# Kernel tuning notes

Hardware: AMD Instinct MI355X
Metric: run time of the kernel (lower is better)

Reference implementation:

```python
import jax, jax.numpy as jnp
import numpy as np

B, S, D = 4, 2048, 1024
H = 16
HD = D // H  # head_dim = 64


def setup_inputs() -> dict:
    key = jax.random.key(0)
    ks = jax.random.split(key, 8)
    scale = 1.0 / np.sqrt(D)
    return {
        "X_Q": jax.random.normal(ks[0], (B, S, D), dtype=jnp.float32),
        "X_KV": jax.random.normal(ks[1], (B, S, D), dtype=jnp.float32),
        # q_proj: Linear(D, D), weights stored as (in, out)
        "q_w": jax.random.normal(ks[2], (D, D), dtype=jnp.float32) * scale,
        "q_b": jax.random.normal(ks[3], (D,), dtype=jnp.float32) * scale,
        # kv_proj: Linear(D, 2*D)
        "kv_w": jax.random.normal(ks[4], (D, 2 * D), dtype=jnp.float32) * scale,
        "kv_b": jax.random.normal(ks[5], (2 * D,), dtype=jnp.float32) * scale,
        # out_proj: Linear(D, D) (query_dim == input_dim)
        "out_w": jax.random.normal(ks[6], (D, D), dtype=jnp.float32) * scale,
        "out_b": jax.random.normal(ks[7], (D,), dtype=jnp.float32) * scale,
    }


def reference(X_Q, X_KV, q_w, q_b, kv_w, kv_b, out_w, out_b):
    # projections
    q = X_Q @ q_w + q_b                      # [b, s, D]
    kv = X_KV @ kv_w + kv_b                  # [b, l, 2D]
    k, v = jnp.split(kv, 2, axis=-1)         # each [b, l, D]

    def split_heads(t):
        b, m, _ = t.shape
        return t.reshape(b, m, H, HD).transpose(0, 2, 1, 3)  # [b, h, m, d]

    q, k, v = split_heads(q), split_heads(k), split_heads(v)

    # standard attention: full SxL scores (non-flash path)
    scores = jnp.einsum("bhsd,bhld->bhsl", q, k) / np.sqrt(HD)
    attn = jax.nn.softmax(scores, axis=-1)   # dropout_p = 0 -> identity
    out = jnp.einsum("bhsl,bhld->bhsd", attn, v)

    # merge heads: [b, h, s, d] -> [b, s, h*d]
    out = out.transpose(0, 2, 1, 3).reshape(B, S, D)
    return out @ out_w + out_b
```

## Files before the change

### kernel.cpp

```cpp
#include <hip/hip_runtime.h>
#include <hip/hip_bf16.h>
#include <math.h>

#define B_  4
#define S_  2048
#define D_  1024
#define H_  16
#define HD_ 64

typedef __bf16 bf16;
typedef __bf16 bf16x4 __attribute__((ext_vector_type(4)));
typedef __bf16 bf16x8 __attribute__((ext_vector_type(8)));
typedef float  floatx4 __attribute__((ext_vector_type(4)));

#define QSCALE 0.18033688011112042f

__device__ __forceinline__ void async_load16(const bf16* g, bf16* l) {
  __builtin_amdgcn_global_load_lds(
      (const __attribute__((address_space(1))) void*)g,
      (__attribute__((address_space(3))) void*)l, 16, 0, 0);
}

__global__ __launch_bounds__(256) void prep_all(
    const float* __restrict__ xa, bf16* __restrict__ oa,
    const float* __restrict__ xb, bf16* __restrict__ ob,
    const float* __restrict__ qw, bf16* __restrict__ qwT,
    const float* __restrict__ kvw, bf16* __restrict__ kvwT,
    const float* __restrict__ ow, bf16* __restrict__ owT) {
  __shared__ float tile[32][33];
  int bid = blockIdx.x;
  if (bid < 16384) {
    const float* in; bf16* out; int i;
    if (bid < 8192) { in = xa; out = oa; i = (bid * 256 + threadIdx.x) * 4; }
    else            { in = xb; out = ob; i = ((bid - 8192) * 256 + threadIdx.x) * 4; }
    float4 v = *reinterpret_cast<const float4*>(in + i);
    bf16x4 o;
    o[0] = (bf16)v.x; o[1] = (bf16)v.y; o[2] = (bf16)v.z; o[3] = (bf16)v.w;
    *reinterpret_cast<bf16x4*>(out + i) = o;
    return;
  }
  bid -= 16384;
  const float* in; bf16* out; int N, lb;
  if (bid < 1024)      { in = qw;  out = qwT;  N = 1024; lb = bid; }
  else if (bid < 3072) { in = kvw; out = kvwT; N = 2048; lb = bid - 1024; }
  else                 { in = ow;  out = owT;  N = 1024; lb = bid - 3072; }
  int nx = N >> 5;
  int n0 = (lb % nx) * 32, k0 = (lb / nx) * 32;
  int tx = threadIdx.x & 31, ty = threadIdx.x >> 5;
  #pragma unroll
  for (int i = ty; i < 32; i += 8)
    tile[i][tx] = in[(size_t)(k0 + i) * N + n0 + tx];
  __syncthreads();
  #pragma unroll
  for (int i = ty; i < 32; i += 8)
    out[(size_t)(n0 + i) * 1024 + k0 + tx] = (bf16)tile[tx][i];
}

template <int MODE>
__device__ __forceinline__ void gemm_body(
    const bf16* __restrict__ A, const bf16* __restrict__ Bt,
    const float* __restrict__ bias, void* __restrict__ out,
    int M, int N, int K, int bx, int by,
    bf16 (*As)[64], bf16 (*Bs)[64]) {
  const int tid  = threadIdx.x;
  const int m0   = by * 128;
  const int n0   = bx * 128;
  const int w    = tid >> 6;
  const int lane = tid & 63;
  const int lr   = lane & 15;
  const int lq   = lane >> 4;
  const int wm   = (w >> 1) * 64;
  const int wn   = (w & 1) * 64;

  const int srow = lane >> 3;
  const int sg   = (lane & 7) ^ srow;
  const bf16* aptr = A  + (size_t)(m0 + 32 * w + srow) * K + 8 * sg;
  const bf16* bptr = Bt + (size_t)(n0 + 32 * w + srow) * K + 8 * sg;

  floatx4 acc[4][4];
  #pragma unroll
  for (int i = 0; i < 4; i++)
    #pragma unroll
    for (int j = 0; j < 4; j++)
      acc[i][j] = floatx4{0.f, 0.f, 0.f, 0.f};

  for (int k0 = 0; k0 < K; k0 += 64) {
    __syncthreads();
    #pragma unroll
    for (int p = 0; p < 4; p++) {
      async_load16(aptr + (size_t)8 * p * K + k0, &As[32 * w + 8 * p][0]);
      async_load16(bptr + (size_t)8 * p * K + k0, &Bs[32 * w + 8 * p][0]);
    }
    __syncthreads();
    #pragma unroll
    for (int kc = 0; kc < 2; kc++) {
      const int sw = 8 * ((kc * 4 + lq) ^ (lr & 7));
      bf16x8 af[4], bfv[4];
      #pragma unroll
      for (int t = 0; t < 4; t++)
        af[t] = *reinterpret_cast<const bf16x8*>(&As[wm + 16 * t + lr][sw]);
      #pragma unroll
      for (int t = 0; t < 4; t++)
        bfv[t] = *reinterpret_cast<const bf16x8*>(&Bs[wn + 16 * t + lr][sw]);
      #pragma unroll
      for (int i = 0; i < 4; i++)
        #pragma unroll
        for (int j = 0; j < 4; j++)
          acc[i][j] = __builtin_amdgcn_mfma_f32_16x16x32_bf16(af[i], bfv[j], acc[i][j], 0, 0, 0);
    }
  }

  #pragma unroll
  for (int i = 0; i < 4; i++) {
    int row_base = m0 + wm + 16 * i + lq * 4;
    #pragma unroll
    for (int j = 0; j < 4; j++) {
      int col = n0 + wn + 16 * j + lr;
      float bv = bias[col];
      if (MODE == 2 && col >= 1024) {
        int b = row_base >> 11, s0 = row_base & 2047;
        int c = col - 1024, h = c >> 6, d = c & 63;
        bf16* Vt = (bf16*)out + (size_t)B_ * H_ * S_ * HD_;
        bf16x4 pk;
        #pragma unroll
        for (int r = 0; r < 4; r++) pk[r] = (bf16)(acc[i][j][r] + bv);
        *reinterpret_cast<bf16x4*>(
            &Vt[(((size_t)b * H_ + h) * HD_ + d) * S_ + s0]) = pk;
        continue;
      }
      #pragma unroll
      for (int r = 0; r < 4; r++) {
        int row = row_base + r;
        float v = acc[i][j][r] + bv;
        if (MODE == 0) {
          ((float*)out)[(size_t)row * N + col] = v;
        } else if (MODE == 1) {
          int b = row >> 11, s = row & 2047;
          int h = col >> 6, d = col & 63;
          ((bf16*)out)[(((size_t)b * H_ + h) * S_ + s) * HD_ + d] =
              (bf16)(v * QSCALE);
        } else {
          int b = row >> 11, s = row & 2047;
          int h = col >> 6, d = col & 63;
          ((bf16*)out)[(((size_t)b * H_ + h) * S_ + s) * HD_ + d] = (bf16)v;
        }
      }
    }
  }
}

__global__ __launch_bounds__(256) void gemm_out(
    const bf16* __restrict__ A, const bf16* __restrict__ Bt,
    const float* __restrict__ bias, void* __restrict__ out,
    int M, int N, int K) {
  __shared__ bf16 As[128][64];
  __shared__ bf16 Bs[128][64];
  gemm_body<0>(A, Bt, bias, out, M, N, K, blockIdx.x, blockIdx.y, As, Bs);
}

__global__ __launch_bounds__(256) void gemm_qkv(
    const bf16* __restrict__ Xq, const bf16* __restrict__ qwT,
    const float* __restrict__ q_b, bf16* __restrict__ Qb,
    const bf16* __restrict__ Xkv, const bf16* __restrict__ kvwT,
    const float* __restrict__ kv_b, bf16* __restrict__ KVb) {
  __shared__ bf16 As[128][64];
  __shared__ bf16 Bs[128][64];
  int bid = blockIdx.x;
  if (bid < 512) {
    gemm_body<1>(Xq, qwT, q_b, Qb, 8192, 1024, 1024, bid & 7, bid >> 3, As, Bs);
  } else {
    int b2 = bid - 512;
    gemm_body<2>(Xkv, kvwT, kv_b, KVb, 8192, 2048, 1024, b2 & 15, b2 >> 4, As, Bs);
  }
}

__global__ __launch_bounds__(256, 2) void attn_kernel(
    const bf16* __restrict__ Q, const bf16* __restrict__ Kb,
    const bf16* __restrict__ Vt, bf16* __restrict__ out) {
  __shared__ bf16 smem[8192];

  const int tid  = threadIdx.x;
  const int w    = tid >> 6;
  const int lane = tid & 63;
  const int lr   = lane & 15;
  const int lq   = lane >> 4;
  const int bh   = blockIdx.x;
  const int q0   = blockIdx.y * 256;
  const size_t base = (size_t)bh * S_ * HD_;

  bf16* pw = smem + w * 2048;

  const bf16* kit = Kb + base + (size_t)lr * HD_ + 8 * lq;
  const bf16* vit = Vt + base + (size_t)lr * S_ + 8 * lq;

  bf16x8 bq[4][2];
  #pragma unroll
  for (int g = 0; g < 4; g++) {
    const bf16* qrow = Q + base + (size_t)(q0 + 64 * w + 16 * g + lr) * HD_;
    bq[g][0] = *reinterpret_cast<const bf16x8*>(qrow + lq * 8);
    bq[g][1] = *reinterpret_cast<const bf16x8*>(qrow + 32 + lq * 8);
  }

  const int plx = lr >> 1;

  float l_i[4] = {0.f, 0.f, 0.f, 0.f};
  floatx4 o_acc[4][4];
  #pragma unroll
  for (int g = 0; g < 4; g++)
    #pragma unroll
    for (int t = 0; t < 4; t++) o_acc[g][t] = floatx4{0.f, 0.f, 0.f, 0.f};

  const int NIT = S_ / 64;
  for (int it = 0; it < NIT; it++) {
    auto qkt = [&](int t) {
      bf16x8 ak0 = *reinterpret_cast<const bf16x8*>(kit + 16 * t * HD_);
      bf16x8 ak1 = *reinterpret_cast<const bf16x8*>(kit + 16 * t * HD_ + 32);
      floatx4 sc[4];
      #pragma unroll
      for (int g = 0; g < 4; g++) {
        sc[g] = __builtin_amdgcn_mfma_f32_16x16x32_bf16(ak0, bq[g][0],
                    floatx4{0.f, 0.f, 0.f, 0.f}, 0, 0, 0);
        sc[g] = __builtin_amdgcn_mfma_f32_16x16x32_bf16(ak1, bq[g][1], sc[g], 0, 0, 0);
      }
      const int pcol = 4 * ((4 * (t & 1) + lq) ^ plx);
      #pragma unroll
      for (int g = 0; g < 4; g++) {
        bf16x4 pk;
        float lsum = 0.f;
        #pragma unroll
        for (int r = 0; r < 4; r++) {
          float p = __builtin_amdgcn_exp2f(sc[g][r]);
          lsum += p;
          pk[r] = (bf16)p;
        }
        l_i[g] += lsum;
        *reinterpret_cast<bf16x4*>(&pw[(16 * g + lr) * 32 + pcol]) = pk;
      }
    };

    auto pv = [&](const bf16x8* av) {
      bf16x8 bp[4];
      #pragma unroll
      for (int g = 0; g < 4; g++) {
        union { bf16x4 h[2]; bf16x8 v; } f;
        f.h[0] = *reinterpret_cast<const bf16x4*>(
            &pw[(16 * g + lr) * 32 + 4 * ((2 * lq + 0) ^ plx)]);
        f.h[1] = *reinterpret_cast<const bf16x4*>(
            &pw[(16 * g + lr) * 32 + 4 * ((2 * lq + 1) ^ plx)]);
        bp[g] = f.v;
      }
      __builtin_amdgcn_s_setprio(1);
      #pragma unroll
      for (int t2 = 0; t2 < 4; t2++)
        #pragma unroll
        for (int g = 0; g < 4; g++)
          o_acc[g][t2] = __builtin_amdgcn_mfma_f32_16x16x32_bf16(av[t2], bp[g], o_acc[g][t2], 0, 0, 0);
      __builtin_amdgcn_s_setprio(0);
    };

    bf16x8 av0[4];
    #pragma unroll
    for (int t2 = 0; t2 < 4; t2++)
      av0[t2] = *reinterpret_cast<const bf16x8*>(vit + (size_t)16 * t2 * S_);
    qkt(0);
    qkt(1);
    __builtin_amdgcn_wave_barrier();
    pv(av0);
    __builtin_amdgcn_wave_barrier();
    bf16x8 av1[4];
    #pragma unroll
    for (int t2 = 0; t2 < 4; t2++)
      av1[t2] = *reinterpret_cast<const bf16x8*>(vit + (size_t)16 * t2 * S_ + 32);
    qkt(2);
    qkt(3);
    __builtin_amdgcn_wave_barrier();
    pv(av1);

    kit += 64 * HD_;
    vit += 64;
  }

  #pragma unroll
  for (int g = 0; g < 4; g++) {
    l_i[g] += __shfl_xor(l_i[g], 16, 64);
    l_i[g] += __shfl_xor(l_i[g], 32, 64);
  }

  const int b = bh >> 4, h = bh & 15;
  #pragma unroll
  for (int g = 0; g < 4; g++) {
    const float inv = 1.0f / l_i[g];
    const int qrow = q0 + 64 * w + 16 * g + lr;
    bf16* orow = out + ((size_t)b * S_ + qrow) * D_ + h * HD_;
    #pragma unroll
    for (int t = 0; t < 4; t++) {
      bf16x4 pk;
      #pragma unroll
      for (int r = 0; r < 4; r++) pk[r] = (bf16)(o_acc[g][t][r] * inv);
      *reinterpret_cast<bf16x4*>(&orow[16 * t + lq * 4]) = pk;
    }
  }
}

extern "C" void kernel_launch(void* const* d_in, const int* in_sizes, int n_in,
                              void* d_out, int out_size, void* d_ws, size_t ws_size,
                              hipStream_t stream) {
  const float* X_Q   = (const float*)d_in[0];
  const float* X_KV  = (const float*)d_in[1];
  const float* q_w   = (const float*)d_in[2];
  const float* q_b   = (const float*)d_in[3];
  const float* kv_w  = (const float*)d_in[4];
  const float* kv_b  = (const float*)d_in[5];
  const float* out_w = (const float*)d_in[6];
  const float* out_b = (const float*)d_in[7];
  float* out = (float*)d_out;

  char* ws = (char*)d_ws;
  const size_t MB = 1024 * 1024;
  bf16* Xq   = (bf16*)(ws + 0);
  bf16* Xkv  = (bf16*)(ws + 16 * MB);
  bf16* Qb   = (bf16*)(ws + 32 * MB);
  bf16* Kb   = (bf16*)(ws + 48 * MB);
  bf16* qwT  = (bf16*)(ws + 80 * MB);
  bf16* kvwT = (bf16*)(ws + 82 * MB);
  bf16* owT  = (bf16*)(ws + 86 * MB);
  bf16* Vt   = Kb + (size_t)B_ * H_ * S_ * HD_;
  bf16* attn = Xq;

  prep_all<<<20480, 256, 0, stream>>>(X_Q, Xq, X_KV, Xkv,
                                      q_w, qwT, kv_w, kvwT, out_w, owT);
  gemm_qkv<<<1536, 256, 0, stream>>>(Xq, qwT, q_b, Qb, Xkv, kvwT, kv_b, Kb);
  attn_kernel<<<dim3(64, 8), 256, 0, stream>>>(Qb, Kb, Vt, attn);
  gemm_out<<<dim3(8, 64), 256, 0, stream>>>(attn, owT, out_b, out, 8192, 1024, 1024);
}
```

Measured before the change: 343.7 us.

## Prefetch K tiles into registers and swap MFMA operands for vectorized GEMM stores

The attention loop now loads the next iteration's K fragments into a second register set while computing on the current one, hiding global load latency behind the QK^T and PV MFMAs. The GEMMs gain a SWAP mode that exchanges the MFMA operands, so each lane holds four consecutive output columns. The epilogue can then use a vector bias load and 16-byte float or 8-byte bf16 stores instead of scalar writes. The cost is extra registers in the attention kernel, which could reduce occupancy under the 2-block launch bound.

```diff
diff --git a/kernel.cpp b/kernel.cpp
--- a/kernel.cpp
+++ b/kernel.cpp
@@ -56,7 +56,7 @@
     out[(size_t)(n0 + i) * 1024 + k0 + tx] = (bf16)tile[tx][i];
 }
 
-template <int MODE>
+template <int MODE, bool SWAP>
 __device__ __forceinline__ void gemm_body(
     const bf16* __restrict__ A, const bf16* __restrict__ Bt,
     const float* __restrict__ bias, void* __restrict__ out,
@@ -105,9 +105,41 @@
       #pragma unroll
       for (int i = 0; i < 4; i++)
         #pragma unroll
-        for (int j = 0; j < 4; j++)
-          acc[i][j] = __builtin_amdgcn_mfma_f32_16x16x32_bf16(af[i], bfv[j], acc[i][j], 0, 0, 0);
-    }
+        for (int j = 0; j < 4; j++) {
+          if (SWAP)
+            acc[i][j] = __builtin_amdgcn_mfma_f32_16x16x32_bf16(bfv[i], af[j], acc[i][j], 0, 0, 0);
+          else
+            acc[i][j] = __builtin_amdgcn_mfma_f32_16x16x32_bf16(af[i], bfv[j], acc[i][j], 0, 0, 0);
+        }
+    }
+  }
+
+  if (SWAP) {
+    #pragma unroll
+    for (int i = 0; i < 4; i++) {
+      const int colb = n0 + wn + 16 * i + 4 * lq;
+      const floatx4 bv4 = *reinterpret_cast<const floatx4*>(&bias[colb]);
+      #pragma unroll
+      for (int j = 0; j < 4; j++) {
+        const int row = m0 + wm + 16 * j + lr;
+        if (MODE == 0) {
+          floatx4 v = acc[i][j] + bv4;
+          *reinterpret_cast<floatx4*>(&((float*)out)[(size_t)row * N + colb]) = v;
+        } else {
+          const int b = row >> 11, s = row & 2047;
+          const int h = colb >> 6, d0 = colb & 63;
+          bf16x4 pk;
+          #pragma unroll
+          for (int r = 0; r < 4; r++) {
+            float v = acc[i][j][r] + bv4[r];
+            pk[r] = (bf16)(MODE == 1 ? v * QSCALE : v);
+          }
+          *reinterpret_cast<bf16x4*>(
+              &((bf16*)out)[(((size_t)b * H_ + h) * S_ + s) * HD_ + d0]) = pk;
+        }
+      }
+    }
+    return;
   }
 
   #pragma unroll
@@ -134,15 +166,11 @@
         float v = acc[i][j][r] + bv;
         if (MODE == 0) {
           ((float*)out)[(size_t)row * N + col] = v;
-        } else if (MODE == 1) {
+        } else {
           int b = row >> 11, s = row & 2047;
           int h = col >> 6, d = col & 63;
           ((bf16*)out)[(((size_t)b * H_ + h) * S_ + s) * HD_ + d] =
-              (bf16)(v * QSCALE);
-        } else {
-          int b = row >> 11, s = row & 2047;
-          int h = col >> 6, d = col & 63;
-          ((bf16*)out)[(((size_t)b * H_ + h) * S_ + s) * HD_ + d] = (bf16)v;
+              (bf16)(MODE == 1 ? v * QSCALE : v);
         }
       }
     }
@@ -155,7 +183,7 @@
     int M, int N, int K) {
   __shared__ bf16 As[128][64];
   __shared__ bf16 Bs[128][64];
-  gemm_body<0>(A, Bt, bias, out, M, N, K, blockIdx.x, blockIdx.y, As, Bs);
+  gemm_body<0, true>(A, Bt, bias, out, M, N, K, blockIdx.x, blockIdx.y, As, Bs);
 }
 
 __global__ __launch_bounds__(256) void gemm_qkv(
@@ -167,10 +195,14 @@
   __shared__ bf16 Bs[128][64];
   int bid = blockIdx.x;
   if (bid < 512) {
-    gemm_body<1>(Xq, qwT, q_b, Qb, 8192, 1024, 1024, bid & 7, bid >> 3, As, Bs);
+    gemm_body<1, true>(Xq, qwT, q_b, Qb, 8192, 1024, 1024, bid & 7, bid >> 3, As, Bs);
   } else {
     int b2 = bid - 512;
-    gemm_body<2>(Xkv, kvwT, kv_b, KVb, 8192, 2048, 1024, b2 & 15, b2 >> 4, As, Bs);
+    int bx = b2 & 15, by = b2 >> 4;
+    if (bx < 8)
+      gemm_body<2, true>(Xkv, kvwT, kv_b, KVb, 8192, 2048, 1024, bx, by, As, Bs);
+    else
+      gemm_body<2, false>(Xkv, kvwT, kv_b, KVb, 8192, 2048, 1024, bx, by, As, Bs);
   }
 }
 
@@ -211,16 +243,32 @@
     for (int t = 0; t < 4; t++) o_acc[g][t] = floatx4{0.f, 0.f, 0.f, 0.f};
 
   const int NIT = S_ / 64;
-  for (int it = 0; it < NIT; it++) {
+
+  bf16x8 kA[8], kB[8];
+  #pragma unroll
+  for (int t = 0; t < 4; t++) {
+    kA[2 * t]     = *reinterpret_cast<const bf16x8*>(kit + 16 * t * HD_);
+    kA[2 * t + 1] = *reinterpret_cast<const bf16x8*>(kit + 16 * t * HD_ + 32);
+  }
+  kit += 64 * HD_;
+
+  auto body = [&](bf16x8 (&cur)[8], bf16x8 (&nxt)[8], int it) {
+    if (it + 1 < NIT) {
+      #pragma unroll
+      for (int t = 0; t < 4; t++) {
+        nxt[2 * t]     = *reinterpret_cast<const bf16x8*>(kit + 16 * t * HD_);
+        nxt[2 * t + 1] = *reinterpret_cast<const bf16x8*>(kit + 16 * t * HD_ + 32);
+      }
+      kit += 64 * HD_;
+    }
+
     auto qkt = [&](int t) {
-      bf16x8 ak0 = *reinterpret_cast<const bf16x8*>(kit + 16 * t * HD_);
-      bf16x8 ak1 = *reinterpret_cast<const bf16x8*>(kit + 16 * t * HD_ + 32);
       floatx4 sc[4];
       #pragma unroll
       for (int g = 0; g < 4; g++) {
-        sc[g] = __builtin_amdgcn_mfma_f32_16x16x32_bf16(ak0, bq[g][0],
+        sc[g] = __builtin_amdgcn_mfma_f32_16x16x32_bf16(cur[2 * t], bq[g][0],
                     floatx4{0.f, 0.f, 0.f, 0.f}, 0, 0, 0);
-        sc[g] = __builtin_amdgcn_mfma_f32_16x16x32_bf16(ak1, bq[g][1], sc[g], 0, 0, 0);
+        sc[g] = __builtin_amdgcn_mfma_f32_16x16x32_bf16(cur[2 * t + 1], bq[g][1], sc[g], 0, 0, 0);
       }
       const int pcol = 4 * ((4 * (t & 1) + lq) ^ plx);
       #pragma unroll
@@ -276,8 +324,12 @@
     __builtin_amdgcn_wave_barrier();
     pv(av1);
 
-    kit += 64 * HD_;
     vit += 64;
+  };
+
+  for (int it = 0; it < NIT; it += 2) {
+    body(kA, kB, it);
+    body(kB, kA, it + 1);
   }
 
   #pragma unroll
```

After: 419.8 us. 22.1% more time.

## Split attention keys across two wave groups with LDS-staged double-buffered K

Applied to the files above, without the earlier changes.

The attention block grows to 512 threads. Two groups of four waves each handle half of the key sequence for the same 256 queries, and their partial outputs and row sums are merged through shared memory at the end. K tiles are now loaded into LDS with async global-to-LDS copies, using an XOR swizzle and double buffering, instead of being read directly from global memory into registers. This adds parallelism within each block and overlaps the K loads with compute. The cost is a block-wide barrier every iteration, much more shared memory per block (which may lower occupancy), and an extra reduction phase.

```diff
diff --git a/kernel.cpp b/kernel.cpp
--- a/kernel.cpp
+++ b/kernel.cpp
@@ -174,33 +174,46 @@
   }
 }
 
-__global__ __launch_bounds__(256, 2) void attn_kernel(
+__global__ __launch_bounds__(512, 2) void attn_kernel(
     const bf16* __restrict__ Q, const bf16* __restrict__ Kb,
     const bf16* __restrict__ Vt, bf16* __restrict__ out) {
-  __shared__ bf16 smem[8192];
+  __shared__ bf16 smem[32768];
 
   const int tid  = threadIdx.x;
   const int w    = tid >> 6;
+  const int wl   = w & 3;
+  const int grp  = w >> 2;
   const int lane = tid & 63;
   const int lr   = lane & 15;
   const int lq   = lane >> 4;
   const int bh   = blockIdx.x;
   const int q0   = blockIdx.y * 256;
   const size_t base = (size_t)bh * S_ * HD_;
-
-  bf16* pw = smem + w * 2048;
-
-  const bf16* kit = Kb + base + (size_t)lr * HD_ + 8 * lq;
-  const bf16* vit = Vt + base + (size_t)lr * S_ + 8 * lq;
+  const int koff = grp << 10;
+
+  bf16* kdb = smem + grp * 8192;
+  bf16* pw  = smem + 16384 + w * 2048;
+
+  const int srow = lane >> 3;
+  const int sg   = (lane & 7) ^ srow;
+
+  const bf16* kptr = Kb + base + (size_t)(koff + 16 * wl + srow) * HD_ + 8 * sg;
+  const bf16* vit  = Vt + base + (size_t)lr * S_ + koff + 8 * lq;
+
+  #pragma unroll
+  for (int p = 0; p < 2; p++)
+    async_load16(kptr + (size_t)8 * p * HD_, kdb + (16 * wl + 8 * p) * 64);
 
   bf16x8 bq[4][2];
   #pragma unroll
   for (int g = 0; g < 4; g++) {
-    const bf16* qrow = Q + base + (size_t)(q0 + 64 * w + 16 * g + lr) * HD_;
+    const bf16* qrow = Q + base + (size_t)(q0 + 64 * wl + 16 * g + lr) * HD_;
     bq[g][0] = *reinterpret_cast<const bf16x8*>(qrow + lq * 8);
     bq[g][1] = *reinterpret_cast<const bf16x8*>(qrow + 32 + lq * 8);
   }
 
+  const int sw0 = 8 * ((0 + lq) ^ (lr & 7));
+  const int sw1 = 8 * ((4 + lq) ^ (lr & 7));
   const int plx = lr >> 1;
 
   float l_i[4] = {0.f, 0.f, 0.f, 0.f};
@@ -210,11 +223,25 @@
     #pragma unroll
     for (int t = 0; t < 4; t++) o_acc[g][t] = floatx4{0.f, 0.f, 0.f, 0.f};
 
-  const int NIT = S_ / 64;
+  __syncthreads();
+
+  const bf16* kpf = kptr + (size_t)64 * HD_;
+
+  const int NIT = 16;
   for (int it = 0; it < NIT; it++) {
+    bf16* ks = kdb + (it & 1) * 4096;
+
+    if (it + 1 < NIT) {
+      bf16* ksn = kdb + ((it + 1) & 1) * 4096;
+      #pragma unroll
+      for (int p = 0; p < 2; p++)
+        async_load16(kpf + (size_t)8 * p * HD_, ksn + (16 * wl + 8 * p) * 64);
+      kpf += (size_t)64 * HD_;
+    }
+
     auto qkt = [&](int t) {
-      bf16x8 ak0 = *reinterpret_cast<const bf16x8*>(kit + 16 * t * HD_);
-      bf16x8 ak1 = *reinterpret_cast<const bf16x8*>(kit + 16 * t * HD_ + 32);
+      bf16x8 ak0 = *reinterpret_cast<const bf16x8*>(ks + (16 * t + lr) * 64 + sw0);
+      bf16x8 ak1 = *reinterpret_cast<const bf16x8*>(ks + (16 * t + lr) * 64 + sw1);
       floatx4 sc[4];
       #pragma unroll
       for (int g = 0; g < 4; g++) {
@@ -276,28 +303,67 @@
     __builtin_amdgcn_wave_barrier();
     pv(av1);
 
-    kit += 64 * HD_;
     vit += 64;
-  }
-
-  #pragma unroll
-  for (int g = 0; g < 4; g++) {
-    l_i[g] += __shfl_xor(l_i[g], 16, 64);
-    l_i[g] += __shfl_xor(l_i[g], 32, 64);
-  }
-
-  const int b = bh >> 4, h = bh & 15;
-  #pragma unroll
-  for (int g = 0; g < 4; g++) {
-    const float inv = 1.0f / l_i[g];
-    const int qrow = q0 + 64 * w + 16 * g + lr;
-    bf16* orow = out + ((size_t)b * S_ + qrow) * D_ + h * HD_;
-    #pragma unroll
-    for (int t = 0; t < 4; t++) {
-      bf16x4 pk;
-      #pragma unroll
-      for (int r = 0; r < 4; r++) pk[r] = (bf16)(o_acc[g][t][r] * inv);
-      *reinterpret_cast<bf16x4*>(&orow[16 * t + lq * 4]) = pk;
+    __syncthreads();
+  }
+
+  float* red = (float*)smem;
+  const int idx = tid & 255;
+  if (grp == 1) {
+    #pragma unroll
+    for (int g = 0; g < 2; g++)
+      #pragma unroll
+      for (int t = 0; t < 4; t++)
+        *reinterpret_cast<floatx4*>(red + (g * 4 + t) * 1024 + idx * 4) = o_acc[g][t];
+    *reinterpret_cast<floatx4*>(red + 8192 + idx * 4) =
+        floatx4{l_i[0], l_i[1], l_i[2], l_i[3]};
+  }
+  __syncthreads();
+  if (grp == 0) {
+    #pragma unroll
+    for (int g = 0; g < 2; g++)
+      #pragma unroll
+      for (int t = 0; t < 4; t++)
+        o_acc[g][t] += *reinterpret_cast<const floatx4*>(red + (g * 4 + t) * 1024 + idx * 4);
+    floatx4 lv = *reinterpret_cast<const floatx4*>(red + 8192 + idx * 4);
+    #pragma unroll
+    for (int g = 0; g < 4; g++) l_i[g] += lv[g];
+  }
+  __syncthreads();
+  if (grp == 1) {
+    #pragma unroll
+    for (int g = 2; g < 4; g++)
+      #pragma unroll
+      for (int t = 0; t < 4; t++)
+        *reinterpret_cast<floatx4*>(red + ((g - 2) * 4 + t) * 1024 + idx * 4) = o_acc[g][t];
+  }
+  __syncthreads();
+  if (grp == 0) {
+    #pragma unroll
+    for (int g = 2; g < 4; g++)
+      #pragma unroll
+      for (int t = 0; t < 4; t++)
+        o_acc[g][t] += *reinterpret_cast<const floatx4*>(red + ((g - 2) * 4 + t) * 1024 + idx * 4);
+
+    #pragma unroll
+    for (int g = 0; g < 4; g++) {
+      l_i[g] += __shfl_xor(l_i[g], 16, 64);
+      l_i[g] += __shfl_xor(l_i[g], 32, 64);
+    }
+
+    const int b = bh >> 4, h = bh & 15;
+    #pragma unroll
+    for (int g = 0; g < 4; g++) {
+      const float inv = 1.0f / l_i[g];
+      const int qrow = q0 + 64 * wl + 16 * g + lr;
+      bf16* orow = out + ((size_t)b * S_ + qrow) * D_ + h * HD_;
+      #pragma unroll
+      for (int t = 0; t < 4; t++) {
+        bf16x4 pk;
+        #pragma unroll
+        for (int r = 0; r < 4; r++) pk[r] = (bf16)(o_acc[g][t][r] * inv);
+        *reinterpret_cast<bf16x4*>(&orow[16 * t + lq * 4]) = pk;
+      }
     }
   }
 }
@@ -330,6 +396,6 @@
   prep_all<<<20480, 256, 0, stream>>>(X_Q, Xq, X_KV, Xkv,
                                       q_w, qwT, kv_w, kvwT, out_w, owT);
   gemm_qkv<<<1536, 256, 0, stream>>>(Xq, qwT, q_b, Qb, Xkv, kvwT, kv_b, Kb);
-  attn_kernel<<<dim3(64, 8), 256, 0, stream>>>(Qb, Kb, Vt, attn);
+  attn_kernel<<<dim3(64, 8), 512, 0, stream>>>(Qb, Kb, Vt, attn);
   gemm_out<<<dim3(8, 64), 256, 0, stream>>>(attn, owT, out_b, out, 8192, 1024, 1024);
 }
```

After: 318.6 us. -7.3%, faster.
